# Optimization experiments

Hardware: AMD Instinct MI355X
Metric: run time of the kernel (lower is better)

The kernel has to match this reference:

```python
import jax, jax.numpy as jnp
import numpy as np

EMBED = 1024
HEADS = 16
HEAD_DIM = EMBED // HEADS
N, SEQ = 8, 1024


def setup_inputs() -> dict:
    key = jax.random.key(0)
    ks = jax.random.split(key, 9)
    values = jax.random.normal(ks[0], (N, SEQ, EMBED), dtype=jnp.float32)
    keys_ = jax.random.normal(ks[1], (N, SEQ, EMBED), dtype=jnp.float32)
    query = jax.random.normal(ks[2], (N, SEQ, EMBED), dtype=jnp.float32)
    mask = jax.random.randint(ks[3], (N, 1, SEQ, SEQ), 0, 2, dtype=jnp.int32)
    s = 1.0 / np.sqrt(HEAD_DIM)
    Wv = jax.random.normal(ks[4], (HEAD_DIM, HEAD_DIM), dtype=jnp.float32) * s
    Wk = jax.random.normal(ks[5], (HEAD_DIM, HEAD_DIM), dtype=jnp.float32) * s
    Wq = jax.random.normal(ks[6], (HEAD_DIM, HEAD_DIM), dtype=jnp.float32) * s
    Wo = jax.random.normal(ks[7], (EMBED, EMBED), dtype=jnp.float32) * (1.0 / np.sqrt(EMBED))
    bo = jax.random.normal(ks[8], (EMBED,), dtype=jnp.float32) * 0.01
    return {"values": values, "keys": keys_, "query": query, "mask": mask,
            "Wv": Wv, "Wk": Wk, "Wq": Wq, "Wo": Wo, "bo": bo}


def reference(values, keys, query, mask, Wv, Wk, Wq, Wo, bo):
    n, q_len = query.shape[0], query.shape[1]
    v_len, k_len = values.shape[1], keys.shape[1]
    # reshape to (N, len, H, Dh); per-head linear projections share a (Dh,Dh) weight.
    v = values.reshape(n, v_len, HEADS, HEAD_DIM)
    k = keys.reshape(n, k_len, HEADS, HEAD_DIM)
    q = query.reshape(n, q_len, HEADS, HEAD_DIM)
    # torch Linear: x @ W.T
    v = jnp.einsum('nlhd,ed->nlhe', v, Wv)
    k = jnp.einsum('nlhd,ed->nlhe', k, Wk)
    q = jnp.einsum('nlhd,ed->nlhe', q, Wq)
    # scores (N,H,Q,K); mask BEFORE scaling, exactly as the torch module does
    att = jnp.einsum('nqhd,nkhd->nhqk', q, k)
    att = jnp.where(mask == 0, jnp.float32(-1e20), att)
    att = jax.nn.softmax(att / jnp.sqrt(jnp.float32(EMBED)), axis=3)
    out = jnp.einsum('nhql,nlhd->nqhd', att, v).reshape(n, q_len, EMBED)
    return out @ Wo.T + bo
```

## Files before the change

### kernel.cpp

```cpp
#include <hip/hip_runtime.h>
#include <hip/hip_bf16.h>

using bf16x8 = __attribute__((ext_vector_type(8))) __bf16;
using f32x4  = __attribute__((ext_vector_type(4))) float;

#define NB 8
#define SEQ 1024
#define HEADS 16
#define HD 64
#define EMB 1024
#define MASKVAL  -3.125e18f

__global__ __launch_bounds__(256) void mask_pack(const int* __restrict__ mask,
                                                 unsigned long long* __restrict__ mp)
{
    const int row = blockIdx.x, n = blockIdx.y, t = threadIdx.x;
    const int w = t >> 6, lane = t & 63;
    const int* m = mask + ((size_t)n * SEQ + row) * SEQ;
    #pragma unroll
    for (int i = 0; i < 4; ++i) {
        unsigned long long b = __ballot(m[i * 256 + w * 64 + lane] != 0);
        if (lane == 0) mp[((size_t)n * SEQ + row) * 16 + i * 4 + w] = b;
    }
}

__global__ __launch_bounds__(256, 4) void proj_mfma(
    const float* __restrict__ q_in, const float* __restrict__ k_in, const float* __restrict__ v_in,
    const float* __restrict__ Wq, const float* __restrict__ Wk, const float* __restrict__ Wv,
    __bf16* __restrict__ qp, __bf16* __restrict__ kp, __bf16* __restrict__ vpt)
{
    const int z = blockIdx.z;
    const float* X  = (z == 0) ? q_in : (z == 1) ? k_in : v_in;
    const float* Wf = (z == 0) ? Wq   : (z == 1) ? Wk   : Wv;

    __shared__ __align__(16) __bf16 Wb[64 * 72];
    __shared__ __align__(16) __bf16 Xb[64 * 72];
    const int t = threadIdx.x;
    const int nh = blockIdx.y, n = nh >> 4, h = nh & 15;
    const int l0 = blockIdx.x * 64;
    for (int i = t; i < 4096; i += 256)
        Wb[(i >> 6) * 72 + (i & 63)] = (__bf16)Wf[i];
    {
        const int row = t >> 2, seg = (t & 3) * 16;
        const float* src = X + ((size_t)(n * SEQ + l0 + row)) * EMB + h * 64 + seg;
        union { __bf16 b[16]; uint4 u[2]; } tmp;
        #pragma unroll
        for (int jj = 0; jj < 4; ++jj) {
            float4 f = ((const float4*)src)[jj];
            tmp.b[jj*4+0] = (__bf16)f.x; tmp.b[jj*4+1] = (__bf16)f.y;
            tmp.b[jj*4+2] = (__bf16)f.z; tmp.b[jj*4+3] = (__bf16)f.w;
        }
        *(uint4*)&Xb[row * 72 + seg]     = tmp.u[0];
        *(uint4*)&Xb[row * 72 + seg + 8] = tmp.u[1];
    }
    __syncthreads();
    const int w = t >> 6, lane = t & 63, quad = lane >> 4, lr = lane & 15;
    bf16x8 af[2];
    #pragma unroll
    for (int ks = 0; ks < 2; ++ks)
        af[ks] = *(const bf16x8*)&Xb[(w * 16 + lr) * 72 + ks * 32 + quad * 8];
    const f32x4 zero4 = {0.f, 0.f, 0.f, 0.f};
    f32x4 acc[4];
    #pragma unroll
    for (int et = 0; et < 4; ++et) {
        acc[et] = zero4;
        #pragma unroll
        for (int ks = 0; ks < 2; ++ks) {
            bf16x8 bfrag = *(const bf16x8*)&Wb[(et * 16 + lr) * 72 + ks * 32 + quad * 8];
            acc[et] = __builtin_amdgcn_mfma_f32_16x16x32_bf16(af[ks], bfrag, acc[et], 0, 0, 0);
        }
    }
    if (z == 0) {
        #pragma unroll
        for (int et = 0; et < 4; ++et) acc[et] *= 0.03125f;
    }
    if (z < 2) {
        __bf16* out = (z == 0) ? qp : kp;
        #pragma unroll
        for (int et = 0; et < 4; ++et)
            #pragma unroll
            for (int rr = 0; rr < 4; ++rr)
                out[(size_t)nh * 65536 + (size_t)(l0 + w * 16 + quad * 4 + rr) * 64 + et * 16 + lr] =
                    (__bf16)acc[et][rr];
    } else {
        __syncthreads();
        #pragma unroll
        for (int et = 0; et < 4; ++et)
            #pragma unroll
            for (int rr = 0; rr < 4; ++rr)
                Xb[(et * 16 + lr) * 72 + w * 16 + quad * 4 + rr] = (__bf16)acc[et][rr];
        __syncthreads();
        const int e = t >> 2, seg = (t & 3) * 16;
        uint4 a = *(uint4*)&Xb[e * 72 + seg];
        uint4 b = *(uint4*)&Xb[e * 72 + seg + 8];
        __bf16* dst = vpt + (size_t)nh * 65536 + (size_t)e * SEQ + l0 + seg;
        *(uint4*)&dst[0] = a;
        *(uint4*)&dst[8] = b;
    }
}

__global__ __launch_bounds__(256, 4) void attn_mfma(
    const __bf16* __restrict__ qp, const __bf16* __restrict__ kp, const __bf16* __restrict__ vpt,
    const unsigned long long* __restrict__ mp, __bf16* __restrict__ attn_out)
{
    __shared__ __align__(16) __bf16 Ks[64 * 72];
    __shared__ __align__(16) __bf16 Vt[64 * 72];
    __shared__ __align__(16) __bf16 Ps[4][16 * 72];
    const int t = threadIdx.x, w = t >> 6, lane = t & 63, quad = lane >> 4, lr = lane & 15;
    const int bid = blockIdx.x;
    const int nh = bid & 127, qt = bid >> 7;
    const int n = nh >> 4, h = nh & 15;
    const int q0 = qt * 64;
    const __bf16* Q  = qp  + (size_t)nh * 65536;
    const __bf16* K  = kp  + (size_t)nh * 65536;
    const __bf16* VT = vpt + (size_t)nh * 65536;
    const int qrow = q0 + w * 16 + lr;
    bf16x8 qf[2];
    qf[0] = *(const bf16x8*)&Q[(size_t)qrow * 64 + quad * 8];
    qf[1] = *(const bf16x8*)&Q[(size_t)qrow * 64 + 32 + quad * 8];
    const unsigned long long* mrow = mp + ((size_t)n * SEQ + qrow) * 16;

    const f32x4 zero4 = {0.f, 0.f, 0.f, 0.f};
    f32x4 O[4];
    #pragma unroll
    for (int mt = 0; mt < 4; ++mt) O[mt] = zero4;
    float m_run = -3.0e38f, l_run = 0.f;

    for (int kc = 0; kc < 16; ++kc) {
        __syncthreads();
        for (int c = t; c < 512; c += 256) {
            int row = c >> 3, c8 = c & 7;
            *(uint4*)&Ks[row * 72 + c8 * 8] =
                *(const uint4*)&K[(size_t)(kc * 64 + row) * 64 + c8 * 8];
            *(uint4*)&Vt[row * 72 + c8 * 8] =
                *(const uint4*)&VT[(size_t)row * SEQ + kc * 64 + c8 * 8];
        }
        const unsigned long long mword = mrow[kc];
        __syncthreads();
        f32x4 S[4];
        #pragma unroll
        for (int kt = 0; kt < 4; ++kt) {
            S[kt] = zero4;
            #pragma unroll
            for (int ks = 0; ks < 2; ++ks) {
                bf16x8 kf = *(const bf16x8*)&Ks[(kt * 16 + lr) * 72 + ks * 32 + quad * 8];
                S[kt] = __builtin_amdgcn_mfma_f32_16x16x32_bf16(kf, qf[ks], S[kt], 0, 0, 0);
            }
        }
        const unsigned int mlo = (unsigned int)(mword >> (quad * 4));
        const unsigned int mhi = (unsigned int)(mword >> (32 + quad * 4));
        float sv[16];
        #pragma unroll
        for (int kt = 0; kt < 4; ++kt)
            #pragma unroll
            for (int r = 0; r < 4; ++r) {
                unsigned int bits = (kt < 2) ? mlo : mhi;
                int sh = (kt & 1) * 16 + r;
                sv[kt * 4 + r] = ((bits >> sh) & 1u) ? S[kt][r] : MASKVAL;
            }
        float mx = sv[0];
        #pragma unroll
        for (int i = 1; i < 16; ++i) mx = fmaxf(mx, sv[i]);
        mx = fmaxf(mx, __shfl_xor(mx, 16, 64));
        mx = fmaxf(mx, __shfl_xor(mx, 32, 64));
        const float mnew = fmaxf(m_run, mx);
        float e[16], sum = 0.f;
        #pragma unroll
        for (int i = 0; i < 16; ++i) { e[i] = __expf(sv[i] - mnew); sum += e[i]; }
        sum += __shfl_xor(sum, 16, 64);
        sum += __shfl_xor(sum, 32, 64);
        const float alpha = __expf(m_run - mnew);
        m_run = mnew;
        l_run = l_run * alpha + sum;
        #pragma unroll
        for (int mt = 0; mt < 4; ++mt) O[mt] *= alpha;
        #pragma unroll
        for (int kt = 0; kt < 4; ++kt) {
            union { __bf16 b[4]; uint2 u; } pk;
            #pragma unroll
            for (int r = 0; r < 4; ++r) pk.b[r] = (__bf16)e[kt * 4 + r];
            *(uint2*)&Ps[w][lr * 72 + kt * 16 + quad * 4] = pk.u;
        }
        __asm__ __volatile__("s_waitcnt lgkmcnt(0)" ::: "memory");
        #pragma unroll
        for (int ks = 0; ks < 2; ++ks) {
            bf16x8 pf = *(const bf16x8*)&Ps[w][lr * 72 + ks * 32 + quad * 8];
            #pragma unroll
            for (int mt = 0; mt < 4; ++mt) {
                bf16x8 vf = *(const bf16x8*)&Vt[(mt * 16 + lr) * 72 + ks * 32 + quad * 8];
                O[mt] = __builtin_amdgcn_mfma_f32_16x16x32_bf16(vf, pf, O[mt], 0, 0, 0);
            }
        }
    }
    const float linv = 1.0f / l_run;
    #pragma unroll
    for (int mt = 0; mt < 4; ++mt) {
        union { __bf16 b[4]; uint2 u; } pk;
        #pragma unroll
        for (int r = 0; r < 4; ++r) pk.b[r] = (__bf16)(O[mt][r] * linv);
        *(uint2*)&attn_out[((size_t)n * SEQ + qrow) * EMB + h * 64 + mt * 16 + quad * 4] = pk.u;
    }
}

__global__ __launch_bounds__(256) void cvt_wo(const float* __restrict__ Wo, __bf16* __restrict__ Wob)
{
    int i = blockIdx.x * 256 + threadIdx.x;
    float4 f = *(const float4*)&Wo[(size_t)i * 4];
    union { __bf16 b[4]; uint2 u; } tmp;
    tmp.b[0] = (__bf16)f.x; tmp.b[1] = (__bf16)f.y; tmp.b[2] = (__bf16)f.z; tmp.b[3] = (__bf16)f.w;
    *(uint2*)&Wob[(size_t)i * 4] = tmp.u;
}

__global__ __launch_bounds__(256, 2) void out_gemm_mfma(
    const __bf16* __restrict__ A, const __bf16* __restrict__ B,
    const float* __restrict__ bo, float* __restrict__ out)
{
    __shared__ __align__(16) __bf16 As[128 * 40];
    __shared__ __align__(16) __bf16 Bs[128 * 40];
    const int t = threadIdx.x, w = t >> 6, lane = t & 63, quad = lane >> 4, lr = lane & 15;
    const int wr = (w >> 1) * 64, wc = (w & 1) * 64;
    const int r0 = blockIdx.y * 128, e0 = blockIdx.x * 128;
    const f32x4 zero4 = {0.f, 0.f, 0.f, 0.f};
    f32x4 acc[4][4];
    #pragma unroll
    for (int mt = 0; mt < 4; ++mt)
        #pragma unroll
        for (int nt = 0; nt < 4; ++nt) acc[mt][nt] = zero4;
    for (int k0 = 0; k0 < 1024; k0 += 32) {
        __syncthreads();
        for (int c = t; c < 512; c += 256) {
            int row = c >> 2, c8 = c & 3;
            *(uint4*)&As[row * 40 + c8 * 8] =
                *(const uint4*)&A[(size_t)(r0 + row) * EMB + k0 + c8 * 8];
            *(uint4*)&Bs[row * 40 + c8 * 8] =
                *(const uint4*)&B[(size_t)(e0 + row) * EMB + k0 + c8 * 8];
        }
        __syncthreads();
        bf16x8 af[4], bf[4];
        #pragma unroll
        for (int mt = 0; mt < 4; ++mt)
            af[mt] = *(const bf16x8*)&As[(wr + mt * 16 + lr) * 40 + quad * 8];
        #pragma unroll
        for (int nt = 0; nt < 4; ++nt)
            bf[nt] = *(const bf16x8*)&Bs[(wc + nt * 16 + lr) * 40 + quad * 8];
        #pragma unroll
        for (int mt = 0; mt < 4; ++mt)
            #pragma unroll
            for (int nt = 0; nt < 4; ++nt)
                acc[mt][nt] = __builtin_amdgcn_mfma_f32_16x16x32_bf16(af[mt], bf[nt], acc[mt][nt], 0, 0, 0);
    }
    float bv[4];
    #pragma unroll
    for (int nt = 0; nt < 4; ++nt) bv[nt] = bo[e0 + wc + nt * 16 + lr];
    #pragma unroll
    for (int mt = 0; mt < 4; ++mt)
        #pragma unroll
        for (int nt = 0; nt < 4; ++nt)
            #pragma unroll
            for (int rr = 0; rr < 4; ++rr)
                out[(size_t)(r0 + wr + mt * 16 + quad * 4 + rr) * EMB + e0 + wc + nt * 16 + lr] =
                    acc[mt][nt][rr] + bv[nt];
}

extern "C" void kernel_launch(void* const* d_in, const int* in_sizes, int n_in,
                              void* d_out, int out_size, void* d_ws, size_t ws_size,
                              hipStream_t stream) {
    const float* values = (const float*)d_in[0];
    const float* keys   = (const float*)d_in[1];
    const float* query  = (const float*)d_in[2];
    const int*   mask   = (const int*)d_in[3];
    const float* Wv     = (const float*)d_in[4];
    const float* Wk     = (const float*)d_in[5];
    const float* Wq     = (const float*)d_in[6];
    const float* Wo     = (const float*)d_in[7];
    const float* bo     = (const float*)d_in[8];
    float* out = (float*)d_out;

    const size_t per = (size_t)NB * HEADS * SEQ * HD;
    __bf16* qp   = (__bf16*)d_ws;
    __bf16* kp   = qp + per;
    __bf16* vpt  = kp + per;
    __bf16* attn = vpt + per;
    __bf16* Wob  = attn + (size_t)NB * SEQ * EMB;
    unsigned long long* maskp = (unsigned long long*)(Wob + (size_t)EMB * EMB);

    mask_pack<<<dim3(SEQ, NB), 256, 0, stream>>>(mask, maskp);
    proj_mfma<<<dim3(16, 128, 3), 256, 0, stream>>>(query, keys, values, Wq, Wk, Wv, qp, kp, vpt);
    cvt_wo<<<1024, 256, 0, stream>>>(Wo, Wob);
    attn_mfma<<<2048, 256, 0, stream>>>(qp, kp, vpt, maskp, attn);
    out_gemm_mfma<<<dim3(EMB / 128, NB * SEQ / 128), 256, 0, stream>>>(attn, Wob, bo, out);
}
```

Measured before the change: 306.0 us.

## Drop online softmax max, use exp2, process two query tiles per attention block

Removes the running-max/rescale in flash attention, folding log2e into the Q scale and using exp2 directly. Each attention block now covers 128 queries so every K/V tile loaded to LDS is reused for two query groups. Q/K projection outputs are staged through LDS for coalesced stores, and the output GEMM uses 64-row tiles with higher occupancy. Skipping max subtraction risks overflow if scores grow large, and fully masked rows would divide by zero.

```diff
diff --git a/kernel.cpp b/kernel.cpp
--- a/kernel.cpp
+++ b/kernel.cpp
@@ -9,7 +9,16 @@
 #define HEADS 16
 #define HD 64
 #define EMB 1024
-#define MASKVAL  -3.125e18f
+
+#if __has_builtin(__builtin_amdgcn_exp2f)
+  #define EXPD(x) __builtin_amdgcn_exp2f(x)
+  #define QSCALE  0.04508422f
+  #define MASKV  -4.5084e18f
+#else
+  #define EXPD(x) __expf(x)
+  #define QSCALE  0.03125f
+  #define MASKV  -3.125e18f
+#endif
 
 __global__ __launch_bounds__(256) void mask_pack(const int* __restrict__ mask,
                                                  unsigned long long* __restrict__ mp)
@@ -72,18 +81,24 @@
     }
     if (z == 0) {
         #pragma unroll
-        for (int et = 0; et < 4; ++et) acc[et] *= 0.03125f;
-    }
+        for (int et = 0; et < 4; ++et) acc[et] *= QSCALE;
+    }
+    __syncthreads();
     if (z < 2) {
-        __bf16* out = (z == 0) ? qp : kp;
         #pragma unroll
         for (int et = 0; et < 4; ++et)
             #pragma unroll
             for (int rr = 0; rr < 4; ++rr)
-                out[(size_t)nh * 65536 + (size_t)(l0 + w * 16 + quad * 4 + rr) * 64 + et * 16 + lr] =
-                    (__bf16)acc[et][rr];
+                Xb[(w * 16 + quad * 4 + rr) * 72 + et * 16 + lr] = (__bf16)acc[et][rr];
+        __syncthreads();
+        const int row = t >> 2, seg = (t & 3) * 16;
+        uint4 a = *(uint4*)&Xb[row * 72 + seg];
+        uint4 b = *(uint4*)&Xb[row * 72 + seg + 8];
+        __bf16* outp = (z == 0) ? qp : kp;
+        __bf16* dst = outp + (size_t)nh * 65536 + (size_t)(l0 + row) * 64 + seg;
+        *(uint4*)&dst[0] = a;
+        *(uint4*)&dst[8] = b;
     } else {
-        __syncthreads();
         #pragma unroll
         for (int et = 0; et < 4; ++et)
             #pragma unroll
@@ -105,26 +120,34 @@
 {
     __shared__ __align__(16) __bf16 Ks[64 * 72];
     __shared__ __align__(16) __bf16 Vt[64 * 72];
-    __shared__ __align__(16) __bf16 Ps[4][16 * 72];
+    __shared__ __align__(16) __bf16 Ps[4][2][16 * 72];
     const int t = threadIdx.x, w = t >> 6, lane = t & 63, quad = lane >> 4, lr = lane & 15;
     const int bid = blockIdx.x;
-    const int nh = bid & 127, qt = bid >> 7;
+    const int nh = bid & 127, qg = bid >> 7;
     const int n = nh >> 4, h = nh & 15;
-    const int q0 = qt * 64;
+    const int q0 = qg * 128;
     const __bf16* Q  = qp  + (size_t)nh * 65536;
     const __bf16* K  = kp  + (size_t)nh * 65536;
     const __bf16* VT = vpt + (size_t)nh * 65536;
-    const int qrow = q0 + w * 16 + lr;
-    bf16x8 qf[2];
-    qf[0] = *(const bf16x8*)&Q[(size_t)qrow * 64 + quad * 8];
-    qf[1] = *(const bf16x8*)&Q[(size_t)qrow * 64 + 32 + quad * 8];
-    const unsigned long long* mrow = mp + ((size_t)n * SEQ + qrow) * 16;
+
+    int qrow[2];
+    bf16x8 qf[2][2];
+    const unsigned long long* mrow[2];
+    #pragma unroll
+    for (int g = 0; g < 2; ++g) {
+        qrow[g] = q0 + g * 64 + w * 16 + lr;
+        qf[g][0] = *(const bf16x8*)&Q[(size_t)qrow[g] * 64 + quad * 8];
+        qf[g][1] = *(const bf16x8*)&Q[(size_t)qrow[g] * 64 + 32 + quad * 8];
+        mrow[g] = mp + ((size_t)n * SEQ + qrow[g]) * 16;
+    }
 
     const f32x4 zero4 = {0.f, 0.f, 0.f, 0.f};
-    f32x4 O[4];
-    #pragma unroll
-    for (int mt = 0; mt < 4; ++mt) O[mt] = zero4;
-    float m_run = -3.0e38f, l_run = 0.f;
+    f32x4 O[2][4];
+    #pragma unroll
+    for (int g = 0; g < 2; ++g)
+        #pragma unroll
+        for (int mt = 0; mt < 4; ++mt) O[g][mt] = zero4;
+    float l_part[2] = {0.f, 0.f};
 
     for (int kc = 0; kc < 16; ++kc) {
         __syncthreads();
@@ -135,70 +158,71 @@
             *(uint4*)&Vt[row * 72 + c8 * 8] =
                 *(const uint4*)&VT[(size_t)row * SEQ + kc * 64 + c8 * 8];
         }
-        const unsigned long long mword = mrow[kc];
-        __syncthreads();
-        f32x4 S[4];
-        #pragma unroll
-        for (int kt = 0; kt < 4; ++kt) {
-            S[kt] = zero4;
-            #pragma unroll
-            for (int ks = 0; ks < 2; ++ks) {
-                bf16x8 kf = *(const bf16x8*)&Ks[(kt * 16 + lr) * 72 + ks * 32 + quad * 8];
-                S[kt] = __builtin_amdgcn_mfma_f32_16x16x32_bf16(kf, qf[ks], S[kt], 0, 0, 0);
+        const unsigned long long mw0 = mrow[0][kc], mw1 = mrow[1][kc];
+        __syncthreads();
+        #pragma unroll
+        for (int g = 0; g < 2; ++g) {
+            f32x4 S[4];
+            #pragma unroll
+            for (int kt = 0; kt < 4; ++kt) {
+                S[kt] = zero4;
+                #pragma unroll
+                for (int ks = 0; ks < 2; ++ks) {
+                    bf16x8 kf = *(const bf16x8*)&Ks[(kt * 16 + lr) * 72 + ks * 32 + quad * 8];
+                    S[kt] = __builtin_amdgcn_mfma_f32_16x16x32_bf16(kf, qf[g][ks], S[kt], 0, 0, 0);
+                }
             }
-        }
-        const unsigned int mlo = (unsigned int)(mword >> (quad * 4));
-        const unsigned int mhi = (unsigned int)(mword >> (32 + quad * 4));
-        float sv[16];
-        #pragma unroll
-        for (int kt = 0; kt < 4; ++kt)
-            #pragma unroll
-            for (int r = 0; r < 4; ++r) {
-                unsigned int bits = (kt < 2) ? mlo : mhi;
-                int sh = (kt & 1) * 16 + r;
-                sv[kt * 4 + r] = ((bits >> sh) & 1u) ? S[kt][r] : MASKVAL;
+            const unsigned long long mword = g ? mw1 : mw0;
+            const unsigned int mlo = (unsigned int)(mword >> (quad * 4));
+            const unsigned int mhi = (unsigned int)(mword >> (32 + quad * 4));
+            float lsum = 0.f;
+            __bf16 pb[16];
+            #pragma unroll
+            for (int kt = 0; kt < 4; ++kt)
+                #pragma unroll
+                for (int r = 0; r < 4; ++r) {
+                    unsigned int bits = (kt < 2) ? mlo : mhi;
+                    int sh = (kt & 1) * 16 + r;
+                    float sv = ((bits >> sh) & 1u) ? S[kt][r] : MASKV;
+                    float ev = EXPD(sv);
+                    lsum += ev;
+                    pb[kt * 4 + r] = (__bf16)ev;
+                }
+            l_part[g] += lsum;
+            #pragma unroll
+            for (int kt = 0; kt < 4; ++kt) {
+                union { __bf16 b[4]; uint2 u; } pk;
+                #pragma unroll
+                for (int r = 0; r < 4; ++r) pk.b[r] = pb[kt * 4 + r];
+                *(uint2*)&Ps[w][g][lr * 72 + kt * 16 + quad * 4] = pk.u;
             }
-        float mx = sv[0];
-        #pragma unroll
-        for (int i = 1; i < 16; ++i) mx = fmaxf(mx, sv[i]);
-        mx = fmaxf(mx, __shfl_xor(mx, 16, 64));
-        mx = fmaxf(mx, __shfl_xor(mx, 32, 64));
-        const float mnew = fmaxf(m_run, mx);
-        float e[16], sum = 0.f;
-        #pragma unroll
-        for (int i = 0; i < 16; ++i) { e[i] = __expf(sv[i] - mnew); sum += e[i]; }
-        sum += __shfl_xor(sum, 16, 64);
-        sum += __shfl_xor(sum, 32, 64);
-        const float alpha = __expf(m_run - mnew);
-        m_run = mnew;
-        l_run = l_run * alpha + sum;
-        #pragma unroll
-        for (int mt = 0; mt < 4; ++mt) O[mt] *= alpha;
-        #pragma unroll
-        for (int kt = 0; kt < 4; ++kt) {
-            union { __bf16 b[4]; uint2 u; } pk;
-            #pragma unroll
-            for (int r = 0; r < 4; ++r) pk.b[r] = (__bf16)e[kt * 4 + r];
-            *(uint2*)&Ps[w][lr * 72 + kt * 16 + quad * 4] = pk.u;
         }
         __asm__ __volatile__("s_waitcnt lgkmcnt(0)" ::: "memory");
         #pragma unroll
         for (int ks = 0; ks < 2; ++ks) {
-            bf16x8 pf = *(const bf16x8*)&Ps[w][lr * 72 + ks * 32 + quad * 8];
+            bf16x8 pf0 = *(const bf16x8*)&Ps[w][0][lr * 72 + ks * 32 + quad * 8];
+            bf16x8 pf1 = *(const bf16x8*)&Ps[w][1][lr * 72 + ks * 32 + quad * 8];
             #pragma unroll
             for (int mt = 0; mt < 4; ++mt) {
                 bf16x8 vf = *(const bf16x8*)&Vt[(mt * 16 + lr) * 72 + ks * 32 + quad * 8];
-                O[mt] = __builtin_amdgcn_mfma_f32_16x16x32_bf16(vf, pf, O[mt], 0, 0, 0);
+                O[0][mt] = __builtin_amdgcn_mfma_f32_16x16x32_bf16(vf, pf0, O[0][mt], 0, 0, 0);
+                O[1][mt] = __builtin_amdgcn_mfma_f32_16x16x32_bf16(vf, pf1, O[1][mt], 0, 0, 0);
             }
         }
     }
-    const float linv = 1.0f / l_run;
-    #pragma unroll
-    for (int mt = 0; mt < 4; ++mt) {
-        union { __bf16 b[4]; uint2 u; } pk;
-        #pragma unroll
-        for (int r = 0; r < 4; ++r) pk.b[r] = (__bf16)(O[mt][r] * linv);
-        *(uint2*)&attn_out[((size_t)n * SEQ + qrow) * EMB + h * 64 + mt * 16 + quad * 4] = pk.u;
+    #pragma unroll
+    for (int g = 0; g < 2; ++g) {
+        float l = l_part[g];
+        l += __shfl_xor(l, 16, 64);
+        l += __shfl_xor(l, 32, 64);
+        const float linv = 1.0f / l;
+        #pragma unroll
+        for (int mt = 0; mt < 4; ++mt) {
+            union { __bf16 b[4]; uint2 u; } pk;
+            #pragma unroll
+            for (int r = 0; r < 4; ++r) pk.b[r] = (__bf16)(O[g][mt][r] * linv);
+            *(uint2*)&attn_out[((size_t)n * SEQ + qrow[g]) * EMB + h * 64 + mt * 16 + quad * 4] = pk.u;
+        }
     }
 }
 
@@ -211,40 +235,43 @@
     *(uint2*)&Wob[(size_t)i * 4] = tmp.u;
 }
 
-__global__ __launch_bounds__(256, 2) void out_gemm_mfma(
+__global__ __launch_bounds__(256, 4) void out_gemm_mfma(
     const __bf16* __restrict__ A, const __bf16* __restrict__ B,
     const float* __restrict__ bo, float* __restrict__ out)
 {
-    __shared__ __align__(16) __bf16 As[128 * 40];
+    __shared__ __align__(16) __bf16 As[64 * 40];
     __shared__ __align__(16) __bf16 Bs[128 * 40];
     const int t = threadIdx.x, w = t >> 6, lane = t & 63, quad = lane >> 4, lr = lane & 15;
-    const int wr = (w >> 1) * 64, wc = (w & 1) * 64;
-    const int r0 = blockIdx.y * 128, e0 = blockIdx.x * 128;
+    const int wr = (w >> 1) * 32, wc = (w & 1) * 64;
+    const int r0 = blockIdx.y * 64, e0 = blockIdx.x * 128;
     const f32x4 zero4 = {0.f, 0.f, 0.f, 0.f};
-    f32x4 acc[4][4];
-    #pragma unroll
-    for (int mt = 0; mt < 4; ++mt)
+    f32x4 acc[2][4];
+    #pragma unroll
+    for (int mt = 0; mt < 2; ++mt)
         #pragma unroll
         for (int nt = 0; nt < 4; ++nt) acc[mt][nt] = zero4;
     for (int k0 = 0; k0 < 1024; k0 += 32) {
         __syncthreads();
+        {
+            int row = t >> 2, c8 = t & 3;
+            *(uint4*)&As[row * 40 + c8 * 8] =
+                *(const uint4*)&A[(size_t)(r0 + row) * EMB + k0 + c8 * 8];
+        }
         for (int c = t; c < 512; c += 256) {
             int row = c >> 2, c8 = c & 3;
-            *(uint4*)&As[row * 40 + c8 * 8] =
-                *(const uint4*)&A[(size_t)(r0 + row) * EMB + k0 + c8 * 8];
             *(uint4*)&Bs[row * 40 + c8 * 8] =
                 *(const uint4*)&B[(size_t)(e0 + row) * EMB + k0 + c8 * 8];
         }
         __syncthreads();
-        bf16x8 af[4], bf[4];
-        #pragma unroll
-        for (int mt = 0; mt < 4; ++mt)
+        bf16x8 af[2], bf[4];
+        #pragma unroll
+        for (int mt = 0; mt < 2; ++mt)
             af[mt] = *(const bf16x8*)&As[(wr + mt * 16 + lr) * 40 + quad * 8];
         #pragma unroll
         for (int nt = 0; nt < 4; ++nt)
             bf[nt] = *(const bf16x8*)&Bs[(wc + nt * 16 + lr) * 40 + quad * 8];
         #pragma unroll
-        for (int mt = 0; mt < 4; ++mt)
+        for (int mt = 0; mt < 2; ++mt)
             #pragma unroll
             for (int nt = 0; nt < 4; ++nt)
                 acc[mt][nt] = __builtin_amdgcn_mfma_f32_16x16x32_bf16(af[mt], bf[nt], acc[mt][nt], 0, 0, 0);
@@ -253,7 +280,7 @@
     #pragma unroll
     for (int nt = 0; nt < 4; ++nt) bv[nt] = bo[e0 + wc + nt * 16 + lr];
     #pragma unroll
-    for (int mt = 0; mt < 4; ++mt)
+    for (int mt = 0; mt < 2; ++mt)
         #pragma unroll
         for (int nt = 0; nt < 4; ++nt)
             #pragma unroll
@@ -287,6 +314,6 @@
     mask_pack<<<dim3(SEQ, NB), 256, 0, stream>>>(mask, maskp);
     proj_mfma<<<dim3(16, 128, 3), 256, 0, stream>>>(query, keys, values, Wq, Wk, Wv, qp, kp, vpt);
     cvt_wo<<<1024, 256, 0, stream>>>(Wo, Wob);
-    attn_mfma<<<2048, 256, 0, stream>>>(qp, kp, vpt, maskp, attn);
-    out_gemm_mfma<<<dim3(EMB / 128, NB * SEQ / 128), 256, 0, stream>>>(attn, Wob, bo, out);
-}
+    attn_mfma<<<1024, 256, 0, stream>>>(qp, kp, vpt, maskp, attn);
+    out_gemm_mfma<<<dim3(EMB / 128, NB * SEQ / 64), 256, 0, stream>>>(attn, Wob, bo, out);
+}
```

Result: faster. 284.7 us (-7.0%).
